# Kernel optimization log

Measured on AMD Instinct MI355X. Metric: run time of the kernel, lower is better.

## Reference

```python
import jax, jax.numpy as jnp
import numpy as np

N_NODES = 50000
N_EDGES = 800000
IN_CH = 256
OUT_CH = 64
HEADS = 4


def setup_inputs() -> dict:
    key = jax.random.key(0)
    k1, k2, k3, k4, k5 = jax.random.split(key, 5)
    x = jax.random.normal(k1, (N_NODES, IN_CH), dtype=jnp.float32)
    edge_index = jax.random.randint(k2, (2, N_EDGES), 0, N_NODES, dtype=jnp.int64)
    # xavier-ish scaled params
    weight = jax.random.normal(k3, (HEADS, IN_CH, OUT_CH), dtype=jnp.float32) * (2.0 / (IN_CH + OUT_CH)) ** 0.5
    att_src = jax.random.normal(k4, (1, HEADS, OUT_CH), dtype=jnp.float32) * 0.1
    att_dst = jax.random.normal(k5, (1, HEADS, OUT_CH), dtype=jnp.float32) * 0.1
    bias = jnp.zeros((HEADS * OUT_CH,), dtype=jnp.float32)
    return {"x": x, "edge_index": edge_index, "weight": weight,
            "att_src": att_src, "att_dst": att_dst, "bias": bias}


def reference(x, edge_index, weight, att_src, att_dst, bias):
    # GATConv forward (eval mode: dropout is identity), vectorized over heads.
    num_nodes = x.shape[0]
    row, col = edge_index[0], edge_index[1]
    # per-head projection: [N, H, C]
    x_h = jnp.einsum('nf,hfc->nhc', x, weight)
    alpha_src = jnp.sum(x_h * att_src[0], axis=-1)   # [N, H]
    alpha_dst = jnp.sum(x_h * att_dst[0], axis=-1)   # [N, H]
    alpha = alpha_src[row] + alpha_dst[col]          # [E, H]
    alpha = jax.nn.leaky_relu(alpha, negative_slope=0.2)
    # segment softmax over edges grouped by destination row (numerically stable)
    alpha_max = jax.ops.segment_max(alpha, row, num_segments=num_nodes)  # [N, H]
    alpha = jnp.exp(alpha - alpha_max[row])
    alpha_sum = jax.ops.segment_sum(alpha, row, num_segments=num_nodes)  # [N, H]
    alpha = alpha / jnp.clip(alpha_sum[row], 1e-16)
    # message passing: scatter-add alpha-weighted source features
    messages = alpha[:, :, None] * x_h[col]                              # [E, H, C]
    out = jax.ops.segment_sum(messages, row, num_segments=num_nodes)    # [N, H, C]
    out = out.reshape(num_nodes, -1) + bias                              # concat heads
    return out
```

## Files before the change

### kernel.cpp

```cpp
#include <hip/hip_runtime.h>
#include <math.h>

#define N_IN_CH 256
#define N_OUT   256
#define HEADS   4
#define OUT_CH  64
#define BM      64
#define SCAN_BLOCK 1024

typedef __attribute__((ext_vector_type(8))) short bf16x8;
typedef __attribute__((ext_vector_type(4))) float f32x4;

__device__ __forceinline__ float lrelu(float a) {
  return a >= 0.f ? a : 0.2f * a;
}

__device__ __forceinline__ ushort f2bf(float f) {
  uint u = __float_as_uint(f);
  uint r = (u + 0x7FFFu + ((u >> 16) & 1u)) >> 16;
  return (ushort)r;
}

__device__ __forceinline__ float bflo(uint u) {
  return __uint_as_float((u & 0xFFFFu) << 16);
}
__device__ __forceinline__ float bfhi(uint u) {
  return __uint_as_float(u & 0xFFFF0000u);
}

__global__ void convert_w(const float* __restrict__ w, ushort* __restrict__ bt,
                          int* __restrict__ counts, int nnodes) {
  const int idx = blockIdx.x * 256 + threadIdx.x;
  if (idx < nnodes) counts[idx] = 0;
  const int n = idx >> 8, k = idx & 255;
  const int h = n >> 6, c = n & 63;
  bt[idx] = f2bf(w[h * (N_IN_CH * OUT_CH) + k * OUT_CH + c]);
}

__global__ void count_kernel(const int* __restrict__ row, int* __restrict__ counts,
                             int* __restrict__ rank, int nedges) {
  int e = blockIdx.x * blockDim.x + threadIdx.x;
  if (e < nedges) rank[e] = atomicAdd(&counts[row[e]], 1);
}

__global__ __launch_bounds__(256) void proj_mfma(
    const float* __restrict__ x, const ushort* __restrict__ bt,
    const float* __restrict__ att_src, const float* __restrict__ att_dst,
    ushort* __restrict__ xh, float* __restrict__ asrc, float* __restrict__ adst,
    int nnodes) {
  __shared__ ushort at[BM * N_IN_CH];
  const int tid = threadIdx.x;
  const int wave = tid >> 6;
  const int lane = tid & 63;
  const int n0 = blockIdx.x * BM;

  {
    const int rsub = tid >> 6;
    const int cf = (tid & 63) * 4;
    const int cb = cf * 2;
#pragma unroll
    for (int it = 0; it < 16; ++it) {
      const int row_ = it * 4 + rsub;
      const int grow = n0 + row_;
      float4 xv = make_float4(0.f, 0.f, 0.f, 0.f);
      if (grow < nnodes) xv = *(const float4*)&x[(size_t)grow * N_IN_CH + cf];
      ushort4 b;
      b.x = f2bf(xv.x); b.y = f2bf(xv.y); b.z = f2bf(xv.z); b.w = f2bf(xv.w);
      const int cbs = cb ^ ((row_ & 7) << 4);
      *(ushort4*)((char*)at + row_ * 512 + cbs) = b;
    }
  }
  __syncthreads();

  f32x4 acc[4][4];
#pragma unroll
  for (int mt = 0; mt < 4; ++mt)
#pragma unroll
    for (int nt = 0; nt < 4; ++nt) acc[mt][nt] = (f32x4){0.f, 0.f, 0.f, 0.f};

  const int lmod = lane & 15;
  const int ldiv = lane >> 4;

  for (int ks = 0; ks < 8; ++ks) {
    bf16x8 a[4], b[4];
#pragma unroll
    for (int mt = 0; mt < 4; ++mt) {
      const int row_ = mt * 16 + lmod;
      const int kb = ks * 64 + ldiv * 16;
      const int cbs = kb ^ ((row_ & 7) << 4);
      a[mt] = *(const bf16x8*)((const char*)at + row_ * 512 + cbs);
    }
#pragma unroll
    for (int nt = 0; nt < 4; ++nt) {
      const int n = wave * 64 + nt * 16 + lmod;
      b[nt] = *(const bf16x8*)&bt[(size_t)n * N_IN_CH + ks * 32 + ldiv * 8];
    }
#pragma unroll
    for (int mt = 0; mt < 4; ++mt)
#pragma unroll
      for (int nt = 0; nt < 4; ++nt)
        acc[mt][nt] = __builtin_amdgcn_mfma_f32_16x16x32_bf16(
            a[mt], b[nt], acc[mt][nt], 0, 0, 0);
  }

  float atts[4], attd[4];
#pragma unroll
  for (int nt = 0; nt < 4; ++nt) {
    const int gcol = wave * 64 + nt * 16 + lmod;
    atts[nt] = att_src[gcol];
    attd[nt] = att_dst[gcol];
  }

#pragma unroll
  for (int mt = 0; mt < 4; ++mt) {
#pragma unroll
    for (int reg = 0; reg < 4; ++reg) {
      const int grow = n0 + mt * 16 + ldiv * 4 + reg;
      const bool ok = grow < nnodes;
      float vs = 0.f, vd = 0.f;
#pragma unroll
      for (int nt = 0; nt < 4; ++nt) {
        const float v = acc[mt][nt][reg];
        if (ok) xh[(size_t)grow * N_OUT + wave * 64 + nt * 16 + lmod] = f2bf(v);
        vs = fmaf(v, atts[nt], vs);
        vd = fmaf(v, attd[nt], vd);
      }
#pragma unroll
      for (int d = 1; d < 16; d <<= 1) {
        vs += __shfl_xor(vs, d, 64);
        vd += __shfl_xor(vd, d, 64);
      }
      if (lmod == 0 && ok) {
        asrc[grow * HEADS + wave] = vs;
        adst[grow * HEADS + wave] = vd;
      }
    }
  }
}

__global__ __launch_bounds__(SCAN_BLOCK) void scan1_kernel(
    const int* __restrict__ counts, int* __restrict__ offsets,
    int* __restrict__ partials, int n) {
  __shared__ int wsum[16];
  const int tid = threadIdx.x;
  const int lane = tid & 63;
  const int wid = tid >> 6;
  const int i = blockIdx.x * SCAN_BLOCK + tid;
  int v = (i < n) ? counts[i] : 0;
  int incl = v;
#pragma unroll
  for (int d = 1; d < 64; d <<= 1) {
    int t = __shfl_up(incl, d, 64);
    if (lane >= d) incl += t;
  }
  if (lane == 63) wsum[wid] = incl;
  __syncthreads();
  if (wid == 0) {
    int wv = (lane < 16) ? wsum[lane] : 0;
#pragma unroll
    for (int d = 1; d < 16; d <<= 1) {
      int t = __shfl_up(wv, d, 64);
      if (lane >= d) wv += t;
    }
    if (lane < 16) wsum[lane] = wv;
  }
  __syncthreads();
  const int wexcl = (wid == 0) ? 0 : wsum[wid - 1];
  if (i <= n) offsets[i] = wexcl + incl - v;
  if (tid == SCAN_BLOCK - 1) partials[blockIdx.x] = wsum[15];
}

__global__ void scan2_kernel(int* __restrict__ partials, int nparts) {
  const int lane = threadIdx.x;
  int v = (lane < nparts) ? partials[lane] : 0;
  int incl = v;
#pragma unroll
  for (int d = 1; d < 64; d <<= 1) {
    int t = __shfl_up(incl, d, 64);
    if (lane >= d) incl += t;
  }
  if (lane < nparts) partials[lane] = incl - v;
}

__global__ void scatter_kernel(const int* __restrict__ row, const int* __restrict__ col,
                               const int* __restrict__ rank,
                               const int* __restrict__ offsets,
                               const int* __restrict__ partials,
                               int* __restrict__ ccol, int nedges) {
  int e = blockIdx.x * blockDim.x + threadIdx.x;
  if (e < nedges) {
    const int r = row[e];
    const int pos = offsets[r] + partials[r >> 10] + rank[e];
    ccol[pos] = col[e];
  }
}

__global__ __launch_bounds__(256) void gather_kernel(
    const int* __restrict__ offsets, const int* __restrict__ partials,
    const int* __restrict__ ccol,
    const float* __restrict__ asrc, const float* __restrict__ adst,
    const ushort* __restrict__ xh, const float* __restrict__ bias,
    float* __restrict__ out, int nnodes) {
  __shared__ float pbuf[4][64 * 4];
  __shared__ int clbuf[4][64];
  const int wv = threadIdx.x >> 6;
  const int lane = threadIdx.x & 63;
  const int n = blockIdx.x * 4 + wv;
  if (n >= nnodes) return;
  const int off = offsets[n] + partials[n >> 10];
  const int end = offsets[n + 1] + partials[(n + 1) >> 10];
  const int deg = end - off;
  const int half = lane >> 5;
  const int ch8 = (lane & 31) * 8;
  const int hh = (lane & 31) >> 3;

  const float4 as4 = *(const float4*)&asrc[n * 4];

  float4 s4 = make_float4(0.f, 0.f, 0.f, 0.f);
  float a0 = 0.f, a1 = 0.f, a2 = 0.f, a3 = 0.f;
  float a4 = 0.f, a5 = 0.f, a6 = 0.f, a7 = 0.f;

  for (int b = 0; b < deg; b += 64) {
    const int cnt = min(64, deg - b);
    float4 p = make_float4(0.f, 0.f, 0.f, 0.f);
    int cl_l = 0;
    if (lane < cnt) {
      cl_l = ccol[off + b + lane];
      const float4 ad = *(const float4*)&adst[cl_l * 4];
      p.x = __expf(lrelu(as4.x + ad.x));
      p.y = __expf(lrelu(as4.y + ad.y));
      p.z = __expf(lrelu(as4.z + ad.z));
      p.w = __expf(lrelu(as4.w + ad.w));
      s4.x += p.x; s4.y += p.y; s4.z += p.z; s4.w += p.w;
    }
    *(float4*)&pbuf[wv][lane * 4] = p;
    clbuf[wv][lane] = cl_l;

    int j = 0;
    for (; j + 8 <= cnt; j += 8) {
      int cq[4];
      float wq[4];
      uint4 xq[4];
#pragma unroll
      for (int q = 0; q < 4; ++q) {
        const int e = j + 2 * q + half;
        cq[q] = clbuf[wv][e];
        wq[q] = pbuf[wv][e * 4 + hh];
      }
#pragma unroll
      for (int q = 0; q < 4; ++q)
        xq[q] = *(const uint4*)&xh[(size_t)cq[q] * N_OUT + ch8];
#pragma unroll
      for (int q = 0; q < 4; ++q) {
        a0 = fmaf(wq[q], bflo(xq[q].x), a0);
        a1 = fmaf(wq[q], bfhi(xq[q].x), a1);
        a2 = fmaf(wq[q], bflo(xq[q].y), a2);
        a3 = fmaf(wq[q], bfhi(xq[q].y), a3);
        a4 = fmaf(wq[q], bflo(xq[q].z), a4);
        a5 = fmaf(wq[q], bfhi(xq[q].z), a5);
        a6 = fmaf(wq[q], bflo(xq[q].w), a6);
        a7 = fmaf(wq[q], bfhi(xq[q].w), a7);
      }
    }
    for (; j < cnt; j += 2) {
      const int e = j + half;
      const bool ok = e < cnt;
      const int c0 = clbuf[wv][ok ? e : j];
      const float w0 = ok ? pbuf[wv][e * 4 + hh] : 0.f;
      const uint4 x0 = *(const uint4*)&xh[(size_t)c0 * N_OUT + ch8];
      a0 = fmaf(w0, bflo(x0.x), a0);
      a1 = fmaf(w0, bfhi(x0.x), a1);
      a2 = fmaf(w0, bflo(x0.y), a2);
      a3 = fmaf(w0, bfhi(x0.y), a3);
      a4 = fmaf(w0, bflo(x0.z), a4);
      a5 = fmaf(w0, bfhi(x0.z), a5);
      a6 = fmaf(w0, bflo(x0.w), a6);
      a7 = fmaf(w0, bfhi(x0.w), a7);
    }
  }

  a0 += __shfl_xor(a0, 32, 64);
  a1 += __shfl_xor(a1, 32, 64);
  a2 += __shfl_xor(a2, 32, 64);
  a3 += __shfl_xor(a3, 32, 64);
  a4 += __shfl_xor(a4, 32, 64);
  a5 += __shfl_xor(a5, 32, 64);
  a6 += __shfl_xor(a6, 32, 64);
  a7 += __shfl_xor(a7, 32, 64);

#pragma unroll
  for (int d = 1; d < 64; d <<= 1) {
    s4.x += __shfl_xor(s4.x, d, 64);
    s4.y += __shfl_xor(s4.y, d, 64);
    s4.z += __shfl_xor(s4.z, d, 64);
    s4.w += __shfl_xor(s4.w, d, 64);
  }
  const float sh = (hh == 0) ? s4.x : (hh == 1) ? s4.y : (hh == 2) ? s4.z : s4.w;
  const float invh = 1.f / fmaxf(sh, 1e-16f);

  const int wch = ch8 + half * 4;
  const float4 b4 = *(const float4*)&bias[wch];
  float4 o;
  o.x = fmaf(half ? a4 : a0, invh, b4.x);
  o.y = fmaf(half ? a5 : a1, invh, b4.y);
  o.z = fmaf(half ? a6 : a2, invh, b4.z);
  o.w = fmaf(half ? a7 : a3, invh, b4.w);
  *(float4*)&out[(size_t)n * N_OUT + wch] = o;
}

extern "C" void kernel_launch(void* const* d_in, const int* in_sizes, int n_in,
                              void* d_out, int out_size, void* d_ws, size_t ws_size,
                              hipStream_t stream) {
  const float* x        = (const float*)d_in[0];
  const int*   edge_idx = (const int*)d_in[1];
  const float* weight   = (const float*)d_in[2];
  const float* att_src  = (const float*)d_in[3];
  const float* att_dst  = (const float*)d_in[4];
  const float* bias     = (const float*)d_in[5];
  float* out = (float*)d_out;

  const int nnodes = in_sizes[0] / N_IN_CH;
  const int nedges = in_sizes[1] / 2;
  const int* row = edge_idx;
  const int* col = edge_idx + nedges;

  char* wsb = (char*)d_ws;
  size_t woff = 0;
  auto alloc = [&](size_t bytes) -> char* {
    char* p = wsb + woff;
    woff += (bytes + 255) & ~(size_t)255;
    return p;
  };
  ushort* xh    = (ushort*)alloc((size_t)nnodes * N_OUT * sizeof(ushort));
  ushort* bt    = (ushort*)alloc((size_t)N_OUT * N_IN_CH * sizeof(ushort));
  float* asrc   = (float*)alloc((size_t)nnodes * HEADS * sizeof(float));
  float* adst   = (float*)alloc((size_t)nnodes * HEADS * sizeof(float));
  int* counts   = (int*)alloc((size_t)nnodes * sizeof(int));
  int* offsets  = (int*)alloc((size_t)(nnodes + 1) * sizeof(int));
  int* partials = (int*)alloc(256 * sizeof(int));
  int* rank     = (int*)alloc((size_t)nedges * sizeof(int));
  int* ccol     = (int*)alloc((size_t)nedges * sizeof(int));

  convert_w<<<256, 256, 0, stream>>>(weight, bt, counts, nnodes);

  const int eblocks = (nedges + 255) / 256;
  count_kernel<<<eblocks, 256, 0, stream>>>(row, counts, rank, nedges);

  const int nblocksA = (nnodes + BM - 1) / BM;
  proj_mfma<<<nblocksA, 256, 0, stream>>>(x, bt, att_src, att_dst,
                                          xh, asrc, adst, nnodes);

  const int nscan = (nnodes + 1 + SCAN_BLOCK - 1) / SCAN_BLOCK;
  scan1_kernel<<<nscan, SCAN_BLOCK, 0, stream>>>(counts, offsets, partials, nnodes);
  scan2_kernel<<<1, 64, 0, stream>>>(partials, nscan);

  scatter_kernel<<<eblocks, 256, 0, stream>>>(row, col, rank, offsets, partials,
                                              ccol, nedges);

  gather_kernel<<<(nnodes + 3) / 4, 256, 0, stream>>>(offsets, partials, ccol,
                                                      asrc, adst, xh, bias, out,
                                                      nnodes);
}
```

Baseline: 166.3 us.

## Broadcast neighbor indices by shuffle and issue eight feature gathers before softmax

The gather kernel now broadcasts each edge's column index with wave shuffles instead of staging it in shared memory, and raises the batch to eight 16-byte feature loads per lane per step. The first batch of loads is issued before the attention-weight exponentials are computed, so that latency overlaps the exp work. The separate tail loop is replaced by predicated loads that return zeros for out-of-range edges. The cost is more live registers, which may lower occupancy, plus wasted lanes on low-degree nodes (average degree is about 16).

Result: no change. 166.2 us (-0.1%).

```diff
diff --git a/kernel.cpp b/kernel.cpp
--- a/kernel.cpp
+++ b/kernel.cpp
@@ -202,7 +202,6 @@
     const ushort* __restrict__ xh, const float* __restrict__ bias,
     float* __restrict__ out, int nnodes) {
   __shared__ float pbuf[4][64 * 4];
-  __shared__ int clbuf[4][64];
   const int wv = threadIdx.x >> 6;
   const int lane = threadIdx.x & 63;
   const int n = blockIdx.x * 4 + wv;
@@ -222,36 +221,40 @@
 
   for (int b = 0; b < deg; b += 64) {
     const int cnt = min(64, deg - b);
-    float4 p = make_float4(0.f, 0.f, 0.f, 0.f);
     int cl_l = 0;
-    if (lane < cnt) {
-      cl_l = ccol[off + b + lane];
-      const float4 ad = *(const float4*)&adst[cl_l * 4];
-      p.x = __expf(lrelu(as4.x + ad.x));
-      p.y = __expf(lrelu(as4.y + ad.y));
-      p.z = __expf(lrelu(as4.z + ad.z));
-      p.w = __expf(lrelu(as4.w + ad.w));
-      s4.x += p.x; s4.y += p.y; s4.z += p.z; s4.w += p.w;
-    }
-    *(float4*)&pbuf[wv][lane * 4] = p;
-    clbuf[wv][lane] = cl_l;
-
-    int j = 0;
-    for (; j + 8 <= cnt; j += 8) {
-      int cq[4];
-      float wq[4];
-      uint4 xq[4];
-#pragma unroll
-      for (int q = 0; q < 4; ++q) {
-        const int e = j + 2 * q + half;
-        cq[q] = clbuf[wv][e];
-        wq[q] = pbuf[wv][e * 4 + hh];
-      }
-#pragma unroll
-      for (int q = 0; q < 4; ++q)
-        xq[q] = *(const uint4*)&xh[(size_t)cq[q] * N_OUT + ch8];
-#pragma unroll
-      for (int q = 0; q < 4; ++q) {
+    if (lane < cnt) cl_l = ccol[off + b + lane];
+
+    for (int j = 0; j < cnt; j += 16) {
+      int cq[8];
+#pragma unroll
+      for (int q = 0; q < 8; ++q) cq[q] = __shfl(cl_l, j + 2 * q + half, 64);
+      uint4 xq[8];
+#pragma unroll
+      for (int q = 0; q < 8; ++q) {
+        const bool okq = (j + 2 * q + half) < cnt;
+        xq[q] = okq ? *(const uint4*)&xh[(size_t)cq[q] * N_OUT + ch8]
+                    : make_uint4(0u, 0u, 0u, 0u);
+      }
+
+      if (j == 0) {
+        float4 p = make_float4(0.f, 0.f, 0.f, 0.f);
+        if (lane < cnt) {
+          const float4 ad = *(const float4*)&adst[cl_l * 4];
+          p.x = __expf(lrelu(as4.x + ad.x));
+          p.y = __expf(lrelu(as4.y + ad.y));
+          p.z = __expf(lrelu(as4.z + ad.z));
+          p.w = __expf(lrelu(as4.w + ad.w));
+          s4.x += p.x; s4.y += p.y; s4.z += p.z; s4.w += p.w;
+        }
+        *(float4*)&pbuf[wv][lane * 4] = p;
+      }
+
+      float wq[8];
+#pragma unroll
+      for (int q = 0; q < 8; ++q) wq[q] = pbuf[wv][(j + 2 * q + half) * 4 + hh];
+
+#pragma unroll
+      for (int q = 0; q < 8; ++q) {
         a0 = fmaf(wq[q], bflo(xq[q].x), a0);
         a1 = fmaf(wq[q], bfhi(xq[q].x), a1);
         a2 = fmaf(wq[q], bflo(xq[q].y), a2);
@@ -261,21 +264,6 @@
         a6 = fmaf(wq[q], bflo(xq[q].w), a6);
         a7 = fmaf(wq[q], bfhi(xq[q].w), a7);
       }
-    }
-    for (; j < cnt; j += 2) {
-      const int e = j + half;
-      const bool ok = e < cnt;
-      const int c0 = clbuf[wv][ok ? e : j];
-      const float w0 = ok ? pbuf[wv][e * 4 + hh] : 0.f;
-      const uint4 x0 = *(const uint4*)&xh[(size_t)c0 * N_OUT + ch8];
-      a0 = fmaf(w0, bflo(x0.x), a0);
-      a1 = fmaf(w0, bfhi(x0.x), a1);
-      a2 = fmaf(w0, bflo(x0.y), a2);
-      a3 = fmaf(w0, bfhi(x0.y), a3);
-      a4 = fmaf(w0, bflo(x0.z), a4);
-      a5 = fmaf(w0, bfhi(x0.z), a5);
-      a6 = fmaf(w0, bflo(x0.w), a6);
-      a7 = fmaf(w0, bfhi(x0.w), a7);
     }
   }
 
```
